# Performance work log

Hardware: AMD Instinct MI355X
Metric: run time of the kernel (lower is better)

Reference implementation:

```python
import jax, jax.numpy as jnp
import numpy as np

TEMPERATURE = 0.07
COS_EPS = 1e-8          # torch F.cosine_similarity eps
MASK_FILL = -9e15       # value used to mask the diagonal


def setup_inputs() -> dict:
    key = jax.random.key(0)
    k1, k2 = jax.random.split(key)
    B, D = 4096, 256
    z_i = jax.random.normal(k1, (B, D), dtype=jnp.float32)
    z_j = jax.random.normal(k2, (B, D), dtype=jnp.float32)
    return {"z_i": z_i, "z_j": z_j}


def reference(z_i, z_j):
    B = z_i.shape[0]
    z = jnp.concatenate([z_i, z_j], axis=0)                 # [2B, D]
    # cosine similarity = normalized-GEMM (same math as broadcasted version)
    norms = jnp.maximum(jnp.linalg.norm(z, axis=-1, keepdims=True), COS_EPS)
    zn = z / norms                                          # [2B, D]
    sim = zn @ zn.T                                         # [2B, 2B]
    # fused diagonal mask + temperature scale
    diag = jnp.eye(2 * B, dtype=bool)
    logits = jnp.where(diag, MASK_FILL, sim) / TEMPERATURE  # [2B, 2B]
    # positive pair labels: row k pairs with row (k+B) mod 2B
    labels = jnp.concatenate([jnp.arange(B, 2 * B), jnp.arange(0, B)])
    logp = jax.nn.log_softmax(logits, axis=-1)
    loss = -jnp.mean(jnp.take_along_axis(logp, labels[:, None], axis=-1))
    return loss
```

## Files before the change

kernel.cpp:

```cpp
#include <hip/hip_runtime.h>
#include <hip/hip_bf16.h>

#define B_ROWS 4096
#define TWOB   8192
#define DIM    256
#define INV_T  14.285714285714286f

#define BM 128
#define BN 128
#define NSTRIP 8
#define CT_PER_STRIP 8
#define NCHUNK 64

typedef __bf16 bf16x8 __attribute__((ext_vector_type(8)));
typedef float  f32x4  __attribute__((ext_vector_type(4)));

__global__ __launch_bounds__(256) void normalize_k(const float* __restrict__ zi,
                                                   const float* __restrict__ zj,
                                                   unsigned short* __restrict__ zn,
                                                   float* __restrict__ loss_acc,
                                                   unsigned int* __restrict__ counter) {
    if (blockIdx.x == 0 && threadIdx.x == 0) {
        loss_acc[0] = 0.0f;
        counter[0]  = 0u;
    }
    int wave = threadIdx.x >> 6;
    int lane = threadIdx.x & 63;
    int row  = blockIdx.x * 4 + wave;
    const float* src = (row < B_ROWS) ? (zi + (size_t)row * DIM)
                                      : (zj + (size_t)(row - B_ROWS) * DIM);
    float4 v = reinterpret_cast<const float4*>(src)[lane];
    float ss = v.x * v.x + v.y * v.y + v.z * v.z + v.w * v.w;
#pragma unroll
    for (int off = 32; off >= 1; off >>= 1) ss += __shfl_xor(ss, off);
    float norm = sqrtf(ss);
    norm = fmaxf(norm, 1e-8f);
    float inv = 1.0f / norm;
    ushort4 o;
    o.x = __builtin_bit_cast(unsigned short, __float2bfloat16(v.x * inv));
    o.y = __builtin_bit_cast(unsigned short, __float2bfloat16(v.y * inv));
    o.z = __builtin_bit_cast(unsigned short, __float2bfloat16(v.z * inv));
    o.w = __builtin_bit_cast(unsigned short, __float2bfloat16(v.w * inv));
    reinterpret_cast<ushort4*>(zn)[(size_t)row * 64 + lane] = o;
}

__global__ __launch_bounds__(256, 2) void ntxent_main(const unsigned short* __restrict__ znu,
                                                      float* __restrict__ pos,
                                                      float* __restrict__ strip_sums) {
    const __bf16* zn = (const __bf16*)znu;
    __shared__ __attribute__((aligned(16))) __bf16 Bs[4][BN * 32];

    const int tid  = threadIdx.x;
    const int wave = tid >> 6;
    const int lane = tid & 63;
    const int wr = wave >> 1, wc = wave & 1;
    const int quad = lane >> 4, lc = lane & 15;
    const int rt    = blockIdx.x;
    const int strip = blockIdx.y;
    const int row0  = rt * BM;
    const int posTile = (rt + 32) & 63;

    bf16x8 areg[4][8];
    {
        const char* abase = (const char*)zn + (size_t)(row0 + wr * 64 + lc) * (DIM * 2) + quad * 16;
#pragma unroll
        for (int mi = 0; mi < 4; ++mi)
#pragma unroll
            for (int kt = 0; kt < 8; ++kt)
                areg[mi][kt] = *(const bf16x8*)(abase + (size_t)mi * 16 * (DIM * 2) + kt * 64);
    }

    int stg_off[2];
#pragma unroll
    for (int t = 0; t < 2; ++t) {
        int c  = (wave * 2 + t) * 64 + lane;
        int m  = c >> 2;
        int kc = (c & 3) ^ ((m & 3) ^ ((m >> 2) & 3));
        stg_off[t] = m * DIM + kc * 8;
    }

    const int sw    = (lc & 3) ^ ((lc >> 2) & 3);
    const int bBase = (wc * 64 + lc) * 64 + ((quad ^ sw) * 16);

#define STAGE(C) do { \
        const int col0_ = (strip * CT_PER_STRIP + ((C) >> 3)) * BN; \
        _Pragma("unroll") \
        for (int t_ = 0; t_ < 2; ++t_) { \
            const int j_ = wave * 2 + t_; \
            const __bf16* gb_ = zn + col0_ * DIM + ((C) & 7) * 32 + stg_off[t_]; \
            __builtin_amdgcn_global_load_lds( \
                (const __attribute__((address_space(1))) void*)gb_, \
                (__attribute__((address_space(3))) void*)((char*)Bs + ((C) & 3) * 8192 + j_ * 1024), 16, 0, 0); \
        } } while (0)

#define KSTEP(T, KT, WAITASM, DOSTAGE) do { \
        WAITASM; \
        __builtin_amdgcn_s_barrier(); \
        __builtin_amdgcn_sched_barrier(0); \
        if (DOSTAGE) STAGE((T) + 3); \
        bf16x8 bfr_[4]; \
        _Pragma("unroll") \
        for (int ni = 0; ni < 4; ++ni) \
            bfr_[ni] = *(const bf16x8*)((const char*)Bs + ((T) & 3) * 8192 + bBase + ni * 1024); \
        __builtin_amdgcn_s_setprio(1); \
        _Pragma("unroll") \
        for (int mi = 0; mi < 4; ++mi) \
            _Pragma("unroll") \
            for (int ni = 0; ni < 4; ++ni) \
                acc[mi][ni] = __builtin_amdgcn_mfma_f32_16x16x32_bf16( \
                    areg[mi][KT], bfr_[ni], acc[mi][ni], 0, 0, 0); \
        __builtin_amdgcn_s_setprio(0); \
    } while (0)

#define VM4 asm volatile("s_waitcnt vmcnt(4)" ::: "memory")
#define VM2 asm volatile("s_waitcnt vmcnt(2)" ::: "memory")
#define VM0 asm volatile("s_waitcnt vmcnt(0)" ::: "memory")

#define EPILOGUE(COLTILE, COL0) do { \
        const bool special_ = ((COLTILE) == rt) || ((COLTILE) == posTile); \
        _Pragma("unroll") \
        for (int mi = 0; mi < 4; ++mi) { \
            _Pragma("unroll") \
            for (int ni = 0; ni < 4; ++ni) { \
                f32x4 a_ = acc[mi][ni]; \
                _Pragma("unroll") \
                for (int r = 0; r < 4; ++r) { \
                    float logit_ = a_[r] * INV_T; \
                    float e_ = __expf(logit_); \
                    if (special_) { \
                        int gr_ = row0 + wr * 64 + mi * 16 + quad * 4 + r; \
                        int gc_ = (COL0) + wc * 64 + ni * 16 + lc; \
                        if (gc_ == ((gr_ + B_ROWS) & (TWOB - 1))) { posv[mi] = logit_; posm[mi] = gr_; } \
                        if (gr_ == gc_) e_ = 0.0f; \
                    } \
                    rsum[mi][r] += e_; \
                } \
            } \
        } } while (0)

    STAGE(0); STAGE(1); STAGE(2);

    float rsum[4][4];
    float posv[4] = {0.f, 0.f, 0.f, 0.f};
    int   posm[4] = {-1, -1, -1, -1};
#pragma unroll
    for (int mi = 0; mi < 4; ++mi)
#pragma unroll
        for (int r = 0; r < 4; ++r) rsum[mi][r] = 0.0f;

    f32x4 acc[4][4];
#pragma unroll 1
    for (int ct = 0; ct < CT_PER_STRIP - 1; ++ct) {
        const int colTile = strip * CT_PER_STRIP + ct;
        const int col0 = colTile * BN;
#pragma unroll
        for (int mi = 0; mi < 4; ++mi)
#pragma unroll
            for (int ni = 0; ni < 4; ++ni) acc[mi][ni] = f32x4{0.f, 0.f, 0.f, 0.f};

        KSTEP(ct * 8 + 0, 0, VM4, 1);
        KSTEP(ct * 8 + 1, 1, VM4, 1);
        KSTEP(ct * 8 + 2, 2, VM4, 1);
        KSTEP(ct * 8 + 3, 3, VM4, 1);
        KSTEP(ct * 8 + 4, 4, VM4, 1);
        KSTEP(ct * 8 + 5, 5, VM4, 1);
        KSTEP(ct * 8 + 6, 6, VM4, 1);
        KSTEP(ct * 8 + 7, 7, VM4, 1);

        EPILOGUE(colTile, col0);
    }
    {
        const int colTile = strip * CT_PER_STRIP + 7;
        const int col0 = colTile * BN;
#pragma unroll
        for (int mi = 0; mi < 4; ++mi)
#pragma unroll
            for (int ni = 0; ni < 4; ++ni) acc[mi][ni] = f32x4{0.f, 0.f, 0.f, 0.f};

        KSTEP(56, 0, VM4, 1);
        KSTEP(57, 1, VM4, 1);
        KSTEP(58, 2, VM4, 1);
        KSTEP(59, 3, VM4, 1);
        KSTEP(60, 4, VM4, 1);
        KSTEP(61, 5, VM4, 0);
        KSTEP(62, 6, VM2, 0);
        KSTEP(63, 7, VM0, 0);

        EPILOGUE(colTile, col0);
    }

#pragma unroll
    for (int mi = 0; mi < 4; ++mi)
        if (posm[mi] >= 0) pos[posm[mi]] = posv[mi];

    __syncthreads();
    float* rowsumL = (float*)Bs;
#pragma unroll
    for (int mi = 0; mi < 4; ++mi) {
#pragma unroll
        for (int r = 0; r < 4; ++r) {
            float v = rsum[mi][r];
            v += __shfl_xor(v, 1);
            v += __shfl_xor(v, 2);
            v += __shfl_xor(v, 4);
            v += __shfl_xor(v, 8);
            if (lc == 0) rowsumL[wc * BM + wr * 64 + mi * 16 + quad * 4 + r] = v;
        }
    }
    __syncthreads();
    if (tid < BM)
        strip_sums[(size_t)strip * TWOB + row0 + tid] = rowsumL[tid] + rowsumL[BM + tid];
}

__global__ __launch_bounds__(256) void finalize_k(const float* __restrict__ strip_sums,
                                                  const float* __restrict__ pos,
                                                  float* __restrict__ loss_acc,
                                                  unsigned int* __restrict__ counter,
                                                  float* __restrict__ out) {
    __shared__ float wsums[4];
    const int tid = threadIdx.x;
    const int r   = blockIdx.x * 256 + tid;
    float s = 0.0f;
#pragma unroll
    for (int st = 0; st < NSTRIP; ++st) s += strip_sums[(size_t)st * TWOB + r];
    float local = logf(s) - pos[r];
#pragma unroll
    for (int off = 32; off >= 1; off >>= 1) local += __shfl_xor(local, off);
    if ((tid & 63) == 0) wsums[tid >> 6] = local;
    __syncthreads();
    if (tid == 0) {
        float bsum = wsums[0] + wsums[1] + wsums[2] + wsums[3];
        atomicAdd(loss_acc, bsum);
        __threadfence();
        unsigned int done = atomicAdd(counter, 1u);
        if (done == gridDim.x - 1) {
            float total = atomicAdd(loss_acc, 0.0f);
            out[0] = total / (float)TWOB;
        }
    }
}

extern "C" void kernel_launch(void* const* d_in, const int* in_sizes, int n_in,
                              void* d_out, int out_size, void* d_ws, size_t ws_size,
                              hipStream_t stream) {
    const float* zi = (const float*)d_in[0];
    const float* zj = (const float*)d_in[1];
    unsigned short* zn = (unsigned short*)d_ws;
    float* pos        = (float*)((char*)d_ws + (size_t)TWOB * DIM * 2);
    float* strip_sums = pos + TWOB;
    float* loss_acc   = strip_sums + (size_t)NSTRIP * TWOB;
    unsigned int* counter = (unsigned int*)(loss_acc + 1);
    float* out = (float*)d_out;

    normalize_k<<<dim3(TWOB / 4), 256, 0, stream>>>(zi, zj, zn, loss_acc, counter);
    ntxent_main<<<dim3(64, NSTRIP), 256, 0, stream>>>(zn, pos, strip_sums);
    finalize_k<<<dim3(TWOB / 256), 256, 0, stream>>>(strip_sums, pos, loss_acc, counter, out);
}
```

Measured before the change: 120.6 us.

## Widen column tile to 256 with 512-thread blocks and stage A through LDS

New measurement: 109.8 us. 1.1x faster.

```diff
diff --git a/kernel.cpp b/kernel.cpp
--- a/kernel.cpp
+++ b/kernel.cpp
@@ -7,10 +7,9 @@
 #define INV_T  14.285714285714286f
 
 #define BM 128
-#define BN 128
-#define NSTRIP 8
+#define BN 256
+#define NSTRIP 4
 #define CT_PER_STRIP 8
-#define NCHUNK 64
 
 typedef __bf16 bf16x8 __attribute__((ext_vector_type(8)));
 typedef float  f32x4  __attribute__((ext_vector_type(4)));
@@ -44,71 +43,81 @@
     reinterpret_cast<ushort4*>(zn)[(size_t)row * 64 + lane] = o;
 }
 
-__global__ __launch_bounds__(256, 2) void ntxent_main(const unsigned short* __restrict__ znu,
+__global__ __launch_bounds__(512, 2) void ntxent_main(const unsigned short* __restrict__ znu,
                                                       float* __restrict__ pos,
                                                       float* __restrict__ strip_sums) {
     const __bf16* zn = (const __bf16*)znu;
+    __shared__ __attribute__((aligned(16))) __bf16 As[8][BM * 32];
     __shared__ __attribute__((aligned(16))) __bf16 Bs[4][BN * 32];
 
     const int tid  = threadIdx.x;
     const int wave = tid >> 6;
     const int lane = tid & 63;
-    const int wr = wave >> 1, wc = wave & 1;
+    const int wr = wave >> 2, wc = wave & 3;
     const int quad = lane >> 4, lc = lane & 15;
     const int rt    = blockIdx.x;
     const int strip = blockIdx.y;
     const int row0  = rt * BM;
-    const int posTile = (rt + 32) & 63;
-
-    bf16x8 areg[4][8];
+    const int diagT = rt >> 1;
+    const int posT  = ((rt >> 1) + 16) & 31;
+
+    int stgA;
     {
-        const char* abase = (const char*)zn + (size_t)(row0 + wr * 64 + lc) * (DIM * 2) + quad * 16;
-#pragma unroll
-        for (int mi = 0; mi < 4; ++mi)
-#pragma unroll
-            for (int kt = 0; kt < 8; ++kt)
-                areg[mi][kt] = *(const bf16x8*)(abase + (size_t)mi * 16 * (DIM * 2) + kt * 64);
-    }
-
-    int stg_off[2];
+        int m  = tid >> 2;
+        int kc = (tid & 3) ^ ((m & 3) ^ ((m >> 2) & 3));
+        stgA = m * DIM + kc * 8;
+    }
+    int stgB[2];
 #pragma unroll
     for (int t = 0; t < 2; ++t) {
         int c  = (wave * 2 + t) * 64 + lane;
         int m  = c >> 2;
         int kc = (c & 3) ^ ((m & 3) ^ ((m >> 2) & 3));
-        stg_off[t] = m * DIM + kc * 8;
-    }
-
-    const int sw    = (lc & 3) ^ ((lc >> 2) & 3);
-    const int bBase = (wc * 64 + lc) * 64 + ((quad ^ sw) * 16);
+        stgB[t] = m * DIM + kc * 8;
+    }
+
+#pragma unroll
+    for (int kt = 0; kt < 8; ++kt) {
+        const __bf16* ga = zn + row0 * DIM + kt * 32 + stgA;
+        __builtin_amdgcn_global_load_lds(
+            (const __attribute__((address_space(1))) void*)ga,
+            (__attribute__((address_space(3))) void*)((char*)As + kt * 8192 + wave * 1024), 16, 0, 0);
+    }
 
 #define STAGE(C) do { \
-        const int col0_ = (strip * CT_PER_STRIP + ((C) >> 3)) * BN; \
+        const int col0_ = (strip * 8 + ((C) >> 3)) * BN; \
         _Pragma("unroll") \
         for (int t_ = 0; t_ < 2; ++t_) { \
             const int j_ = wave * 2 + t_; \
-            const __bf16* gb_ = zn + col0_ * DIM + ((C) & 7) * 32 + stg_off[t_]; \
+            const __bf16* gb_ = zn + col0_ * DIM + ((C) & 7) * 32 + stgB[t_]; \
             __builtin_amdgcn_global_load_lds( \
                 (const __attribute__((address_space(1))) void*)gb_, \
-                (__attribute__((address_space(3))) void*)((char*)Bs + ((C) & 3) * 8192 + j_ * 1024), 16, 0, 0); \
+                (__attribute__((address_space(3))) void*)((char*)Bs + ((C) & 3) * 16384 + j_ * 1024), 16, 0, 0); \
         } } while (0)
 
-#define KSTEP(T, KT, WAITASM, DOSTAGE) do { \
+    const int sw    = (lc & 3) ^ ((lc >> 2) & 3);
+    const int aBase = (wr * 64 + lc) * 64 + ((quad ^ sw) * 16);
+    const int bBase = (wc * 64 + lc) * 64 + ((quad ^ sw) * 16);
+
+#define KSTEP(T, WAITASM, DOSTAGE) do { \
         WAITASM; \
         __builtin_amdgcn_s_barrier(); \
         __builtin_amdgcn_sched_barrier(0); \
         if (DOSTAGE) STAGE((T) + 3); \
-        bf16x8 bfr_[4]; \
+        bf16x8 af_[4], bfr_[4]; \
         _Pragma("unroll") \
         for (int ni = 0; ni < 4; ++ni) \
-            bfr_[ni] = *(const bf16x8*)((const char*)Bs + ((T) & 3) * 8192 + bBase + ni * 1024); \
+            bfr_[ni] = *(const bf16x8*)((const char*)Bs + ((T) & 3) * 16384 + bBase + ni * 1024); \
+        _Pragma("unroll") \
+        for (int mi = 0; mi < 4; ++mi) \
+            af_[mi] = *(const bf16x8*)((const char*)As + ((T) & 7) * 8192 + aBase + mi * 1024); \
         __builtin_amdgcn_s_setprio(1); \
         _Pragma("unroll") \
         for (int mi = 0; mi < 4; ++mi) \
             _Pragma("unroll") \
             for (int ni = 0; ni < 4; ++ni) \
                 acc[mi][ni] = __builtin_amdgcn_mfma_f32_16x16x32_bf16( \
-                    areg[mi][KT], bfr_[ni], acc[mi][ni], 0, 0, 0); \
+                    af_[mi], bfr_[ni], acc[mi][ni], 0, 0, 0); \
         __builtin_amdgcn_s_setprio(0); \
     } while (0)
 
@@ -117,7 +126,7 @@
 #define VM0 asm volatile("s_waitcnt vmcnt(0)" ::: "memory")
 
 #define EPILOGUE(COLTILE, COL0) do { \
-        const bool special_ = ((COLTILE) == rt) || ((COLTILE) == posTile); \
+        const bool special_ = ((COLTILE) == diagT) || ((COLTILE) == posT); \
         _Pragma("unroll") \
         for (int mi = 0; mi < 4; ++mi) { \
             _Pragma("unroll") \
@@ -151,40 +160,40 @@
     f32x4 acc[4][4];
 #pragma unroll 1
     for (int ct = 0; ct < CT_PER_STRIP - 1; ++ct) {
-        const int colTile = strip * CT_PER_STRIP + ct;
+        const int colTile = strip * 8 + ct;
         const int col0 = colTile * BN;
 #pragma unroll
         for (int mi = 0; mi < 4; ++mi)
 #pragma unroll
             for (int ni = 0; ni < 4; ++ni) acc[mi][ni] = f32x4{0.f, 0.f, 0.f, 0.f};
 
-        KSTEP(ct * 8 + 0, 0, VM4, 1);
-        KSTEP(ct * 8 + 1, 1, VM4, 1);
-        KSTEP(ct * 8 + 2, 2, VM4, 1);
-        KSTEP(ct * 8 + 3, 3, VM4, 1);
-        KSTEP(ct * 8 + 4, 4, VM4, 1);
-        KSTEP(ct * 8 + 5, 5, VM4, 1);
-        KSTEP(ct * 8 + 6, 6, VM4, 1);
-        KSTEP(ct * 8 + 7, 7, VM4, 1);
+        KSTEP(ct * 8 + 0, VM4, 1);
+        KSTEP(ct * 8 + 1, VM4, 1);
+        KSTEP(ct * 8 + 2, VM4, 1);
+        KSTEP(ct * 8 + 3, VM4, 1);
+        KSTEP(ct * 8 + 4, VM4, 1);
+        KSTEP(ct * 8 + 5, VM4, 1);
+        KSTEP(ct * 8 + 6, VM4, 1);
+        KSTEP(ct * 8 + 7, VM4, 1);
 
         EPILOGUE(colTile, col0);
     }
     {
-        const int colTile = strip * CT_PER_STRIP + 7;
+        const int colTile = strip * 8 + 7;
         const int col0 = colTile * BN;
 #pragma unroll
         for (int mi = 0; mi < 4; ++mi)
 #pragma unroll
             for (int ni = 0; ni < 4; ++ni) acc[mi][ni] = f32x4{0.f, 0.f, 0.f, 0.f};
 
-        KSTEP(56, 0, VM4, 1);
-        KSTEP(57, 1, VM4, 1);
-        KSTEP(58, 2, VM4, 1);
-        KSTEP(59, 3, VM4, 1);
-        KSTEP(60, 4, VM4, 1);
-        KSTEP(61, 5, VM4, 0);
-        KSTEP(62, 6, VM2, 0);
-        KSTEP(63, 7, VM0, 0);
+        KSTEP(56, VM4, 1);
+        KSTEP(57, VM4, 1);
+        KSTEP(58, VM4, 1);
+        KSTEP(59, VM4, 1);
+        KSTEP(60, VM4, 1);
+        KSTEP(61, VM4, 0);
+        KSTEP(62, VM2, 0);
+        KSTEP(63, VM0, 0);
 
         EPILOGUE(colTile, col0);
     }
@@ -194,7 +203,7 @@
         if (posm[mi] >= 0) pos[posm[mi]] = posv[mi];
 
     __syncthreads();
-    float* rowsumL = (float*)Bs;
+    float* rowsumL = (float*)As;
 #pragma unroll
     for (int mi = 0; mi < 4; ++mi) {
 #pragma unroll
@@ -209,7 +218,8 @@
     }
     __syncthreads();
     if (tid < BM)
-        strip_sums[(size_t)strip * TWOB + row0 + tid] = rowsumL[tid] + rowsumL[BM + tid];
+        strip_sums[(size_t)strip * TWOB + row0 + tid] =
+            rowsumL[tid] + rowsumL[BM + tid] + rowsumL[2 * BM + tid] + rowsumL[3 * BM + tid];
 }
 
 __global__ __launch_bounds__(256) void finalize_k(const float* __restrict__ strip_sums,
@@ -253,6 +263,6 @@
     float* out = (float*)d_out;
 
     normalize_k<<<dim3(TWOB / 4), 256, 0, stream>>>(zi, zj, zn, loss_acc, counter);
-    ntxent_main<<<dim3(64, NSTRIP), 256, 0, stream>>>(zn, pos, strip_sums);
+    ntxent_main<<<dim3(64, NSTRIP), 512, 0, stream>>>(zn, pos, strip_sums);
     finalize_k<<<dim3(TWOB / 256), 256, 0, stream>>>(strip_sums, pos, loss_acc, counter, out);
 }
```
